# Kernel optimization log

Hardware: AMD Instinct MI355X
Metric: run time of the kernel (lower is better)

The kernel has to match this reference:

```python
import jax, jax.numpy as jnp
import numpy as np

EMBED_DIM = 1024
HID = EMBED_DIM // 2
N = 32768
L2_REG = 0.001
BN_EPS = 1e-5


def setup_inputs() -> dict:
    key = jax.random.key(0)
    ks = jax.random.split(key, 8)
    inp = {
        "item_emb": jax.random.normal(ks[0], (N, EMBED_DIM), jnp.float32),
        "pos_item_emb": jax.random.normal(ks[1], (N, EMBED_DIM), jnp.float32),
        "neg_item_emb": jax.random.normal(ks[2], (N, EMBED_DIM), jnp.float32),
        # Linear 1: embed_dim -> embed_dim/2 (xavier_normal init, zero bias)
        "W1": jax.random.normal(ks[3], (HID, EMBED_DIM), jnp.float32) * np.sqrt(2.0 / (EMBED_DIM + HID)),
        "b1": jnp.zeros((HID,), jnp.float32),
        # BatchNorm1d params / running stats (eval-mode semantics)
        "gamma": jnp.ones((HID,), jnp.float32),
        "beta": jnp.zeros((HID,), jnp.float32),
        "run_mean": jnp.zeros((HID,), jnp.float32),
        "run_var": jnp.ones((HID,), jnp.float32),
        # Linear 2: embed_dim/2 -> embed_dim
        "W2": jax.random.normal(ks[4], (EMBED_DIM, HID), jnp.float32) * np.sqrt(2.0 / (EMBED_DIM + HID)),
        "b2": jnp.zeros((EMBED_DIM,), jnp.float32),
    }
    return inp


def _net(x, W1, b1, gamma, beta, run_mean, run_var, W2, b2):
    # Linear -> BatchNorm1d (eval stats) -> LeakyReLU(0.1) -> (Dropout=identity) -> Linear
    h = x @ W1.T + b1                                   # [N, HID]
    h = (h - run_mean) * jax.lax.rsqrt(run_var + BN_EPS) * gamma + beta
    h = jnp.where(h >= 0, h, 0.1 * h)
    return h @ W2.T + b2                                # [N, EMBED_DIM]


def reference(item_emb, pos_item_emb, neg_item_emb,
              W1, b1, gamma, beta, run_mean, run_var, W2, b2):
    net = lambda x: _net(x, W1, b1, gamma, beta, run_mean, run_var, W2, b2)
    anchor_e = net(item_emb)
    pos_e = net(pos_item_emb)
    neg_e = net(neg_item_emb)

    dist_pos = jnp.linalg.norm(anchor_e - pos_e, axis=1)  # [N]
    dist_neg = jnp.linalg.norm(anchor_e - neg_e, axis=1)  # [N]

    # fused replacement of the per-sample python loop
    margins = jnp.where(dist_neg < dist_pos, dist_pos - dist_neg, 0.0)
    margin = jnp.quantile(margins, 0.25)  # Q1, linear interpolation (matches torch)

    loss_triplet = jax.nn.relu(dist_neg ** 2 - dist_pos ** 2 + margin)
    l2 = L2_REG * (jnp.sum(anchor_e ** 2) + jnp.sum(pos_e ** 2) + jnp.sum(neg_e ** 2)) / anchor_e.shape[0]
    return jnp.mean(loss_triplet + l2)
```

## Files before the change

kernel.cpp:

```cpp
#include <hip/hip_runtime.h>

#define NROWS 32768
#define DIM   1024
#define HIDD  512
#define M3    (3*NROWS)

using bf16x8 = __attribute__((ext_vector_type(8))) short;
using f32x4  = __attribute__((ext_vector_type(4))) float;

#define MFMA16(a,b,c) __builtin_amdgcn_mfma_f32_16x16x32_bf16(a,b,c,0,0,0)
#define WAIT_VM(N)  asm volatile("s_waitcnt vmcnt(" #N ")" ::: "memory")
#define WAIT_LGKM0  asm volatile("s_waitcnt lgkmcnt(0)" ::: "memory")
#define MEMFENCE    asm volatile("" ::: "memory")
#define BAR()       __builtin_amdgcn_s_barrier()
#define SCHEDB()    __builtin_amdgcn_sched_barrier(0)
#define SP1()       __builtin_amdgcn_s_setprio(1)
#define SP0()       __builtin_amdgcn_s_setprio(0)

static __device__ __forceinline__ unsigned short f2bf(float f) {
    unsigned u = __float_as_uint(f);
    u += 0x7FFFu + ((u >> 16) & 1u);
    return (unsigned short)(u >> 16);
}
static __device__ __forceinline__ unsigned cvtpk(float a, float b) {
    unsigned r;
    asm("v_cvt_pk_bf16_f32 %0, %1, %2" : "=v"(r) : "v"(a), "v"(b));
    return r;
}
static __device__ __forceinline__ void gload16(const void* gsrc, void* ldst) {
    __builtin_amdgcn_global_load_lds(
        (const __attribute__((address_space(1))) unsigned int*)gsrc,
        (__attribute__((address_space(3))) unsigned int*)ldst,
        16, 0, 0);
}

__global__ __launch_bounds__(256)
void cvt_kernel(const float* __restrict__ src, unsigned short* __restrict__ dst, int n4)
{
    const int i = blockIdx.x * 256 + threadIdx.x;
    if (i < n4) {
        float4 v = reinterpret_cast<const float4*>(src)[i];
        uint2 o;
        o.x = cvtpk(v.x, v.y);
        o.y = cvtpk(v.z, v.w);
        reinterpret_cast<uint2*>(dst)[i] = o;
    }
}

__global__ __launch_bounds__(512, 1)
void gemm1_mfma(const float* __restrict__ x0, const float* __restrict__ x1,
                const float* __restrict__ x2,
                const unsigned short* __restrict__ W1bf,
                const float* __restrict__ b1, const float* __restrict__ gamma,
                const float* __restrict__ beta, const float* __restrict__ rmean,
                const float* __restrict__ rvar,
                unsigned short* __restrict__ h)
{
    __shared__ char smem[131072];
    char* const Ab = smem;
    char* const Bb = smem + 65536;

    const int lin = blockIdx.x;
    const int wgid = (lin & 7) * 96 + (lin >> 3);
    const int cb = wgid & 1;
    const int rb = wgid >> 1;
    const int tid  = threadIdx.x;
    const int lane = tid & 63, w = tid >> 6;
    const int wm = w >> 2, wn = w & 3;
    const int row0 = rb * 256;
    const int s = row0 >> 15;
    const float* x = (s == 0) ? x0 : (s == 1 ? x1 : x2);
    const int rl0 = row0 & (NROWS - 1);
    const int col0 = cb * 256;
    const int l15 = lane & 15, lq = lane >> 4;

    f32x4 acc[8][4] = {};
    float4 aR[8];

    const int arow = tid >> 1, ahalf = tid & 1;
    const float* axsrc = &x[(size_t)(rl0 + arow) * DIM + ahalf * 32];

    auto issueA = [&](int k0) {
        #pragma unroll
        for (int j = 0; j < 8; ++j)
            aR[j] = *reinterpret_cast<const float4*>(axsrc + k0 + j * 4);
    };
    auto issueB = [&](int k0, char* Bdst) {
        #pragma unroll
        for (int i = 0; i < 4; ++i) {
            const int f = i * 512 + tid;
            const int col = f >> 3, c = f & 7;
            gload16(&W1bf[(size_t)(col0 + col) * DIM + k0 + ((c ^ (col & 7)) << 3)],
                    Bdst + f * 16);
        }
    };
    auto writeA = [&](char* Adst) {
        #pragma unroll
        for (int j = 0; j < 4; ++j) {
            uint4 o;
            o.x = cvtpk(aR[2*j].x, aR[2*j].y);
            o.y = cvtpk(aR[2*j].z, aR[2*j].w);
            o.z = cvtpk(aR[2*j+1].x, aR[2*j+1].y);
            o.w = cvtpk(aR[2*j+1].z, aR[2*j+1].w);
            const int cidx = ahalf * 4 + j;
            *reinterpret_cast<uint4*>(Adst + ((arow * 128 + cidx * 16) ^ ((arow & 7) << 4))) = o;
        }
    };
    auto readA = [&](bf16x8 (&a)[4][2], int mh, char* Abase) {
        #pragma unroll
        for (int mm = 0; mm < 4; ++mm) {
            const int row = wm * 128 + (mh * 4 + mm) * 16 + l15;
            const int swz = (row & 7) << 4;
            #pragma unroll
            for (int ks = 0; ks < 2; ++ks)
                a[mm][ks] = *reinterpret_cast<const bf16x8*>(
                    Abase + ((row * 128 + ks * 64 + lq * 16) ^ swz));
        }
    };
    auto readB = [&](bf16x8 (&b)[2][2], int nh, char* Bbase) {
        #pragma unroll
        for (int nn = 0; nn < 2; ++nn) {
            const int col = wn * 64 + (nh * 2 + nn) * 16 + l15;
            const int swz = (col & 7) << 4;
            #pragma unroll
            for (int ks = 0; ks < 2; ++ks)
                b[nn][ks] = *reinterpret_cast<const bf16x8*>(
                    Bbase + ((col * 128 + ks * 64 + lq * 16) ^ swz));
        }
    };

    issueA(0);
    MEMFENCE;
    issueB(0, Bb);
    WAIT_VM(4);
    writeA(Ab);
    WAIT_VM(0);
    WAIT_LGKM0;
    BAR();

    for (int t = 0; t < 16; ++t) {
        char* const Apt = Ab + (t & 1) * 32768;
        char* const Apn = Ab + ((t & 1) ^ 1) * 32768;
        char* const Bpt = Bb + (t & 1) * 32768;
        char* const Bpn = Bb + ((t & 1) ^ 1) * 32768;
        const int kn = ((t < 15) ? (t + 1) : 15) * 64;

        bf16x8 a[4][2], b[2][2], a2[4][2];
        readA(a, 0, Apt);
        readB(b, 0, Bpt);
        issueA(kn);
        MEMFENCE;
        issueB(kn, Bpn);
        BAR(); WAIT_LGKM0; SCHEDB(); SP1();
        #pragma unroll
        for (int mm = 0; mm < 4; ++mm)
            #pragma unroll
            for (int nn = 0; nn < 2; ++nn)
                #pragma unroll
                for (int ks = 0; ks < 2; ++ks)
                    acc[mm][nn] = MFMA16(a[mm][ks], b[nn][ks], acc[mm][nn]);
        SP0(); BAR();
        readB(b, 1, Bpt);
        BAR(); WAIT_LGKM0; SCHEDB(); SP1();
        #pragma unroll
        for (int mm = 0; mm < 4; ++mm)
            #pragma unroll
            for (int nn = 0; nn < 2; ++nn)
                #pragma unroll
                for (int ks = 0; ks < 2; ++ks)
                    acc[mm][2 + nn] = MFMA16(a[mm][ks], b[nn][ks], acc[mm][2 + nn]);
        SP0(); BAR();
        readA(a2, 1, Apt);
        WAIT_VM(4);
        writeA(Apn);
        BAR(); WAIT_LGKM0; SCHEDB(); SP1();
        #pragma unroll
        for (int mm = 0; mm < 4; ++mm)
            #pragma unroll
            for (int nn = 0; nn < 2; ++nn)
                #pragma unroll
                for (int ks = 0; ks < 2; ++ks)
                    acc[4 + mm][2 + nn] = MFMA16(a2[mm][ks], b[nn][ks], acc[4 + mm][2 + nn]);
        SP0(); BAR();
        readB(b, 0, Bpt);
        WAIT_VM(0);
        BAR(); WAIT_LGKM0; SCHEDB(); SP1();
        #pragma unroll
        for (int mm = 0; mm < 4; ++mm)
            #pragma unroll
            for (int nn = 0; nn < 2; ++nn)
                #pragma unroll
                for (int ks = 0; ks < 2; ++ks)
                    acc[4 + mm][nn] = MFMA16(a2[mm][ks], b[nn][ks], acc[4 + mm][nn]);
        SP0(); BAR();
    }

    float Asc[4], Bsc[4];
    #pragma unroll
    for (int nf = 0; nf < 4; ++nf) {
        const int c = col0 + wn * 64 + nf * 16 + l15;
        const float inv = rsqrtf(rvar[c] + 1e-5f);
        Asc[nf] = inv * gamma[c];
        Bsc[nf] = (b1[c] - rmean[c]) * Asc[nf] + beta[c];
    }
    #pragma unroll
    for (int mf = 0; mf < 8; ++mf) {
        const int rbase = row0 + wm * 128 + mf * 16 + lq * 4;
        #pragma unroll
        for (int nf = 0; nf < 4; ++nf) {
            const int c = col0 + wn * 64 + nf * 16 + l15;
            #pragma unroll
            for (int i = 0; i < 4; ++i) {
                float v = fmaf(acc[mf][nf][i], Asc[nf], Bsc[nf]);
                v = (v >= 0.f) ? v : 0.1f * v;
                h[(size_t)(rbase + i) * HIDD + c] = f2bf(v);
            }
        }
    }
}

__global__ __launch_bounds__(512, 1)
void gemm2_mfma(const unsigned short* __restrict__ h,
                const unsigned short* __restrict__ W2bf,
                const float* __restrict__ b2,
                float* __restrict__ pdp, float* __restrict__ pdn,
                float* __restrict__ pl2)
{
    __shared__ char smem[114688];
    char* const Ab = smem;
    char* const Bb = smem + 49152;

    const int lin = blockIdx.x;
    const int wgid = (lin & 7) * 256 + (lin >> 3);
    const int cb = wgid & 3;
    const int rb = wgid >> 2;
    const int tid  = threadIdx.x;
    const int lane = tid & 63, w = tid >> 6;
    const int wm = w >> 2, wn = w & 3;
    const int row0 = rb * 64;
    const int col0 = cb * 256;
    const int l15 = lane & 15, lq = lane >> 4;

    f32x4 acc[6][4] = {};

    auto issueA = [&](int k0, char* Adst) {
        #pragma unroll
        for (int i = 0; i < 3; ++i) {
            const int f = i * 512 + tid;
            const int mrow = f >> 3, c = f & 7;
            const int mf = mrow >> 4, rr = mrow & 15;
            const int ss = mf % 3, rf = mf / 3;
            gload16(&h[((size_t)ss * NROWS + row0 + rf * 16 + rr) * HIDD + k0 + ((c ^ (mrow & 7)) << 3)],
                    Adst + f * 16);
        }
    };
    auto issueB = [&](int k0, char* Bdst) {
        #pragma unroll
        for (int i = 0; i < 4; ++i) {
            const int f = i * 512 + tid;
            const int col = f >> 3, c = f & 7;
            gload16(&W2bf[(size_t)(col0 + col) * HIDD + k0 + ((c ^ (col & 7)) << 3)],
                    Bdst + f * 16);
        }
    };
    auto readA = [&](bf16x8 (&a)[3][2], int mh, char* Abase) {
        #pragma unroll
        for (int mm = 0; mm < 3; ++mm) {
            const int row = (wm * 6 + mh * 3 + mm) * 16 + l15;
            const int swz = (row & 7) << 4;
            #pragma unroll
            for (int ks = 0; ks < 2; ++ks)
                a[mm][ks] = *reinterpret_cast<const bf16x8*>(
                    Abase + ((row * 128 + ks * 64 + lq * 16) ^ swz));
        }
    };
    auto readB = [&](bf16x8 (&b)[2][2], int nh, char* Bbase) {
        #pragma unroll
        for (int nn = 0; nn < 2; ++nn) {
            const int col = wn * 64 + (nh * 2 + nn) * 16 + l15;
            const int swz = (col & 7) << 4;
            #pragma unroll
            for (int ks = 0; ks < 2; ++ks)
                b[nn][ks] = *reinterpret_cast<const bf16x8*>(
                    Bbase + ((col * 128 + ks * 64 + lq * 16) ^ swz));
        }
    };

    issueA(0, Ab);
    MEMFENCE;
    issueB(0, Bb);
    WAIT_VM(0);
    BAR();

    for (int t = 0; t < 8; ++t) {
        char* const Apt = Ab + (t & 1) * 24576;
        char* const Apn = Ab + ((t & 1) ^ 1) * 24576;
        char* const Bpt = Bb + (t & 1) * 32768;
        char* const Bpn = Bb + ((t & 1) ^ 1) * 32768;
        const int kn = ((t < 7) ? (t + 1) : 7) * 64;

        bf16x8 a[3][2], b[2][2], a2[3][2];
        readA(a, 0, Apt);
        readB(b, 0, Bpt);
        issueA(kn, Apn);
        MEMFENCE;
        issueB(kn, Bpn);
        BAR(); WAIT_LGKM0; SCHEDB(); SP1();
        #pragma unroll
        for (int mm = 0; mm < 3; ++mm)
            #pragma unroll
            for (int nn = 0; nn < 2; ++nn)
                #pragma unroll
                for (int ks = 0; ks < 2; ++ks)
                    acc[mm][nn] = MFMA16(a[mm][ks], b[nn][ks], acc[mm][nn]);
        SP0(); BAR();
        readB(b, 1, Bpt);
        BAR(); WAIT_LGKM0; SCHEDB(); SP1();
        #pragma unroll
        for (int mm = 0; mm < 3; ++mm)
            #pragma unroll
            for (int nn = 0; nn < 2; ++nn)
                #pragma unroll
                for (int ks = 0; ks < 2; ++ks)
                    acc[mm][2 + nn] = MFMA16(a[mm][ks], b[nn][ks], acc[mm][2 + nn]);
        SP0(); BAR();
        readA(a2, 1, Apt);
        BAR(); WAIT_LGKM0; SCHEDB(); SP1();
        #pragma unroll
        for (int mm = 0; mm < 3; ++mm)
            #pragma unroll
            for (int nn = 0; nn < 2; ++nn)
                #pragma unroll
                for (int ks = 0; ks < 2; ++ks)
                    acc[3 + mm][2 + nn] = MFMA16(a2[mm][ks], b[nn][ks], acc[3 + mm][2 + nn]);
        SP0(); BAR();
        readB(b, 0, Bpt);
        WAIT_VM(0);
        BAR(); WAIT_LGKM0; SCHEDB(); SP1();
        #pragma unroll
        for (int mm = 0; mm < 3; ++mm)
            #pragma unroll
            for (int nn = 0; nn < 2; ++nn)
                #pragma unroll
                for (int ks = 0; ks < 2; ++ks)
                    acc[3 + mm][nn] = MFMA16(a2[mm][ks], b[nn][ks], acc[3 + mm][nn]);
        SP0(); BAR();
    }

    float b2c[4];
    #pragma unroll
    for (int nf = 0; nf < 4; ++nf) b2c[nf] = b2[col0 + wn * 64 + nf * 16 + l15];
    float l2t = 0.f;
    #pragma unroll
    for (int mh = 0; mh < 2; ++mh) {
        const int rbase = row0 + (wm * 2 + mh) * 16 + lq * 4;
        #pragma unroll
        for (int i = 0; i < 4; ++i) {
            float dp = 0.f, dn = 0.f;
            #pragma unroll
            for (int nf = 0; nf < 4; ++nf) {
                const float ea = acc[mh * 3 + 0][nf][i] + b2c[nf];
                const float ep = acc[mh * 3 + 1][nf][i] + b2c[nf];
                const float en = acc[mh * 3 + 2][nf][i] + b2c[nf];
                dp += (ea - ep) * (ea - ep);
                dn += (ea - en) * (ea - en);
                l2t += ea * ea + ep * ep + en * en;
            }
            #pragma unroll
            for (int mm = 1; mm < 16; mm <<= 1) {
                dp += __shfl_xor(dp, mm);
                dn += __shfl_xor(dn, mm);
            }
            if (l15 == 0) {
                pdp[(size_t)(cb * 4 + wn) * NROWS + rbase + i] = dp;
                pdn[(size_t)(cb * 4 + wn) * NROWS + rbase + i] = dn;
            }
        }
    }
    #pragma unroll
    for (int mm = 1; mm < 64; mm <<= 1) l2t += __shfl_xor(l2t, mm);
    __syncthreads();
    float* const l2red = (float*)smem;
    if (lane == 0) l2red[w] = l2t;
    __syncthreads();
    if (tid == 0) {
        float t = 0.f;
        #pragma unroll
        for (int ww = 0; ww < 8; ++ww) t += l2red[ww];
        pl2[wgid] = t;
    }
}

__global__ __launch_bounds__(256)
void margins_kernel(const float* __restrict__ pdp, const float* __restrict__ pdn,
                    float* __restrict__ margins, float* __restrict__ dd)
{
    const int r = blockIdx.x * 256 + threadIdx.x;
    float dp2 = 0.f, dn2 = 0.f;
    #pragma unroll
    for (int q = 0; q < 16; ++q) {
        dp2 += pdp[(size_t)q * NROWS + r];
        dn2 += pdn[(size_t)q * NROWS + r];
    }
    dd[r] = dn2 - dp2;
    margins[r] = (dn2 < dp2) ? (sqrtf(dp2) - sqrtf(dn2)) : 0.f;
}

__global__ __launch_bounds__(1024)
void final_kernel(const float* __restrict__ pl2, int npl2,
                  const float* __restrict__ margins, const float* __restrict__ dd,
                  float* __restrict__ out)
{
    __shared__ unsigned hist[256];
    __shared__ float warp_red[16];
    __shared__ unsigned sh_prefix;
    __shared__ int sh_k;
    __shared__ float sh_l2;
    const int tid = threadIdx.x;

    float l2 = 0.f;
    for (int i = tid; i < npl2; i += 1024) l2 += pl2[i];
    #pragma unroll
    for (int m = 1; m < 64; m <<= 1) l2 += __shfl_xor(l2, m);
    if ((tid & 63) == 0) warp_red[tid >> 6] = l2;
    __syncthreads();
    if (tid == 0) {
        float t = 0.f;
        for (int w = 0; w < 16; ++w) t += warp_red[w];
        sh_l2 = t;
    }
    __syncthreads();

    float vsel[2];
    for (int sel = 0; sel < 2; ++sel) {
        if (tid == 0) { sh_k = 8191 + sel; sh_prefix = 0u; }
        __syncthreads();
        for (int shift = 24; shift >= 0; shift -= 8) {
            if (tid < 256) hist[tid] = 0u;
            __syncthreads();
            const unsigned prefix = sh_prefix;
            const unsigned mask = (shift == 24) ? 0u : (0xFFFFFFFFu << (shift + 8));
            for (int i = tid; i < NROWS; i += 1024) {
                const unsigned key = __float_as_uint(margins[i]);
                if (((key ^ prefix) & mask) == 0u)
                    atomicAdd(&hist[(key >> shift) & 255u], 1u);
            }
            __syncthreads();
            if (tid == 0) {
                int kk = sh_k;
                unsigned cum = 0; int d = 0;
                for (; d < 256; ++d) {
                    const unsigned c = hist[d];
                    if (cum + c > (unsigned)kk) break;
                    cum += c;
                }
                sh_prefix = prefix | ((unsigned)d << shift);
                sh_k = kk - (int)cum;
            }
            __syncthreads();
        }
        vsel[sel] = __uint_as_float(sh_prefix);
        __syncthreads();
    }
    const float margin = vsel[0] + 0.75f * (vsel[1] - vsel[0]);

    float ssum = 0.f;
    for (int i = tid; i < NROWS; i += 1024) {
        const float t = dd[i] + margin;
        ssum += (t > 0.f) ? t : 0.f;
    }
    #pragma unroll
    for (int m = 1; m < 64; m <<= 1) ssum += __shfl_xor(ssum, m);
    if ((tid & 63) == 0) warp_red[tid >> 6] = ssum;
    __syncthreads();
    if (tid == 0) {
        float S = 0.f;
        for (int w = 0; w < 16; ++w) S += warp_red[w];
        out[0] = S / (float)NROWS + 1e-3f * sh_l2 / (float)NROWS;
    }
}

extern "C" void kernel_launch(void* const* d_in, const int* in_sizes, int n_in,
                              void* d_out, int out_size, void* d_ws, size_t ws_size,
                              hipStream_t stream) {
    (void)in_sizes; (void)n_in; (void)out_size; (void)ws_size;
    const float* item = (const float*)d_in[0];
    const float* pos  = (const float*)d_in[1];
    const float* neg  = (const float*)d_in[2];
    const float* W1   = (const float*)d_in[3];
    const float* b1   = (const float*)d_in[4];
    const float* gam  = (const float*)d_in[5];
    const float* bet  = (const float*)d_in[6];
    const float* rmu  = (const float*)d_in[7];
    const float* rvr  = (const float*)d_in[8];
    const float* W2   = (const float*)d_in[9];
    const float* b2   = (const float*)d_in[10];

    char* ws = (char*)d_ws;
    unsigned short* h = (unsigned short*)ws;
    size_t off = (size_t)M3 * HIDD * sizeof(unsigned short);
    unsigned short* W1bf = (unsigned short*)(ws + off); off += (size_t)HIDD * DIM * 2;
    unsigned short* W2bf = (unsigned short*)(ws + off); off += (size_t)DIM * HIDD * 2;
    float* pdp = (float*)(ws + off); off += (size_t)16 * NROWS * 4;
    float* pdn = (float*)(ws + off); off += (size_t)16 * NROWS * 4;
    float* pl2 = (float*)(ws + off); off += (size_t)2048 * 4;
    float* margins = (float*)(ws + off); off += (size_t)NROWS * 4;
    float* dd = (float*)(ws + off); off += (size_t)NROWS * 4;

    cvt_kernel<<<dim3((HIDD*DIM/4 + 255)/256), 256, 0, stream>>>(W1, W1bf, HIDD*DIM/4);
    cvt_kernel<<<dim3((DIM*HIDD/4 + 255)/256), 256, 0, stream>>>(W2, W2bf, DIM*HIDD/4);
    gemm1_mfma<<<dim3(768), 512, 0, stream>>>(
        item, pos, neg, W1bf, b1, gam, bet, rmu, rvr, h);
    gemm2_mfma<<<dim3(2048), 512, 0, stream>>>(
        h, W2bf, b2, pdp, pdn, pl2);
    margins_kernel<<<dim3(NROWS/256), 256, 0, stream>>>(pdp, pdn, margins, dd);
    final_kernel<<<1, 1024, 0, stream>>>(pl2, 2048, margins, dd, (float*)d_out);
}
```

Before: 501.9 us.

## Shrink GEMM1 tiles to 128x128 with 256 threads and single-pass quantile selection

GEMM1 moves from a 256x256 tile with 512 threads, 128KB double-buffered LDS and an interleaved MFMA schedule to a 128x128 tile with 256 threads, 32KB single-buffered LDS and register prefetch of the next X slice. The operands are swapped so the epilogue writes packed bf16 pairs after reading BN scale/shift from LDS. The aim is higher occupancy and simpler sync, but A/B reuse per block drops and the explicit load/compute overlap is gone. Separately, the final kernel finds the second order statistic for the quantile with one count/min pass instead of a second 4-pass radix select.

Result: faster. 438.9 us (-12.6%).

```diff
diff --git a/kernel.cpp b/kernel.cpp
--- a/kernel.cpp
+++ b/kernel.cpp
@@ -17,11 +17,6 @@
 #define SP1()       __builtin_amdgcn_s_setprio(1)
 #define SP0()       __builtin_amdgcn_s_setprio(0)
 
-static __device__ __forceinline__ unsigned short f2bf(float f) {
-    unsigned u = __float_as_uint(f);
-    u += 0x7FFFu + ((u >> 16) & 1u);
-    return (unsigned short)(u >> 16);
-}
 static __device__ __forceinline__ unsigned cvtpk(float a, float b) {
     unsigned r;
     asm("v_cvt_pk_bf16_f32 %0, %1, %2" : "=v"(r) : "v"(a), "v"(b));
@@ -47,7 +42,7 @@
     }
 }
 
-__global__ __launch_bounds__(512, 1)
+__global__ __launch_bounds__(256)
 void gemm1_mfma(const float* __restrict__ x0, const float* __restrict__ x1,
                 const float* __restrict__ x2,
                 const unsigned short* __restrict__ W1bf,
@@ -56,165 +51,117 @@
                 const float* __restrict__ rvar,
                 unsigned short* __restrict__ h)
 {
-    __shared__ char smem[131072];
-    char* const Ab = smem;
-    char* const Bb = smem + 65536;
+    __shared__ char smem[32768];
+    char* const Xb = smem;
+    char* const Wb = smem + 16384;
 
     const int lin = blockIdx.x;
-    const int wgid = (lin & 7) * 96 + (lin >> 3);
-    const int cb = wgid & 1;
-    const int rb = wgid >> 1;
+    const int wgid = (lin & 7) * 384 + (lin >> 3);
+    const int cb = wgid & 3;
+    const int rb = wgid >> 2;
     const int tid  = threadIdx.x;
     const int lane = tid & 63, w = tid >> 6;
-    const int wm = w >> 2, wn = w & 3;
-    const int row0 = rb * 256;
+    const int wr = w >> 1, wc = w & 1;
+    const int row0 = rb * 128;
     const int s = row0 >> 15;
     const float* x = (s == 0) ? x0 : (s == 1 ? x1 : x2);
     const int rl0 = row0 & (NROWS - 1);
-    const int col0 = cb * 256;
+    const int col0 = cb * 128;
     const int l15 = lane & 15, lq = lane >> 4;
 
-    f32x4 acc[8][4] = {};
+    f32x4 acc[4][4] = {};
     float4 aR[8];
 
-    const int arow = tid >> 1, ahalf = tid & 1;
-    const float* axsrc = &x[(size_t)(rl0 + arow) * DIM + ahalf * 32];
-
-    auto issueA = [&](int k0) {
-        #pragma unroll
-        for (int j = 0; j < 8; ++j)
-            aR[j] = *reinterpret_cast<const float4*>(axsrc + k0 + j * 4);
-    };
-    auto issueB = [&](int k0, char* Bdst) {
-        #pragma unroll
-        for (int i = 0; i < 4; ++i) {
-            const int f = i * 512 + tid;
-            const int col = f >> 3, c = f & 7;
-            gload16(&W1bf[(size_t)(col0 + col) * DIM + k0 + ((c ^ (col & 7)) << 3)],
-                    Bdst + f * 16);
-        }
-    };
-    auto writeA = [&](char* Adst) {
-        #pragma unroll
-        for (int j = 0; j < 4; ++j) {
-            uint4 o;
-            o.x = cvtpk(aR[2*j].x, aR[2*j].y);
-            o.y = cvtpk(aR[2*j].z, aR[2*j].w);
-            o.z = cvtpk(aR[2*j+1].x, aR[2*j+1].y);
-            o.w = cvtpk(aR[2*j+1].z, aR[2*j+1].w);
-            const int cidx = ahalf * 4 + j;
-            *reinterpret_cast<uint4*>(Adst + ((arow * 128 + cidx * 16) ^ ((arow & 7) << 4))) = o;
-        }
-    };
-    auto readA = [&](bf16x8 (&a)[4][2], int mh, char* Abase) {
-        #pragma unroll
-        for (int mm = 0; mm < 4; ++mm) {
-            const int row = wm * 128 + (mh * 4 + mm) * 16 + l15;
-            const int swz = (row & 7) << 4;
-            #pragma unroll
-            for (int ks = 0; ks < 2; ++ks)
-                a[mm][ks] = *reinterpret_cast<const bf16x8*>(
-                    Abase + ((row * 128 + ks * 64 + lq * 16) ^ swz));
-        }
-    };
-    auto readB = [&](bf16x8 (&b)[2][2], int nh, char* Bbase) {
-        #pragma unroll
-        for (int nn = 0; nn < 2; ++nn) {
-            const int col = wn * 64 + (nh * 2 + nn) * 16 + l15;
-            const int swz = (col & 7) << 4;
-            #pragma unroll
-            for (int ks = 0; ks < 2; ++ks)
-                b[nn][ks] = *reinterpret_cast<const bf16x8*>(
-                    Bbase + ((col * 128 + ks * 64 + lq * 16) ^ swz));
-        }
-    };
-
-    issueA(0);
-    MEMFENCE;
-    issueB(0, Bb);
-    WAIT_VM(4);
-    writeA(Ab);
-    WAIT_VM(0);
-    WAIT_LGKM0;
-    BAR();
+    #pragma unroll
+    for (int p = 0; p < 8; ++p) {
+        const int f = p * 256 + tid;
+        const int r = f >> 4, c4 = f & 15;
+        aR[p] = *reinterpret_cast<const float4*>(&x[(size_t)(rl0 + r) * DIM + c4 * 4]);
+    }
 
     for (int t = 0; t < 16; ++t) {
-        char* const Apt = Ab + (t & 1) * 32768;
-        char* const Apn = Ab + ((t & 1) ^ 1) * 32768;
-        char* const Bpt = Bb + (t & 1) * 32768;
-        char* const Bpn = Bb + ((t & 1) ^ 1) * 32768;
-        const int kn = ((t < 15) ? (t + 1) : 15) * 64;
-
-        bf16x8 a[4][2], b[2][2], a2[4][2];
-        readA(a, 0, Apt);
-        readB(b, 0, Bpt);
-        issueA(kn);
-        MEMFENCE;
-        issueB(kn, Bpn);
-        BAR(); WAIT_LGKM0; SCHEDB(); SP1();
-        #pragma unroll
-        for (int mm = 0; mm < 4; ++mm)
-            #pragma unroll
-            for (int nn = 0; nn < 2; ++nn)
+        const int k0 = t * 64;
+        #pragma unroll
+        for (int p = 0; p < 8; ++p) {
+            const int f = p * 256 + tid;
+            const int r = f >> 4, c4 = f & 15;
+            const unsigned off = (unsigned)((r * 128 + c4 * 8) ^ ((r & 7) << 4));
+            uint2 o; o.x = cvtpk(aR[p].x, aR[p].y); o.y = cvtpk(aR[p].z, aR[p].w);
+            *reinterpret_cast<uint2*>(Xb + off) = o;
+        }
+        #pragma unroll
+        for (int c = 0; c < 4; ++c) {
+            const int f = c * 256 + tid;
+            const int panel = f >> 9;
+            const int cc = (f >> 2) & 127;
+            const int chunk = (f & 3) ^ ((cc >> 1) & 3);
+            gload16(&W1bf[(size_t)(col0 + cc) * DIM + k0 + panel * 32 + chunk * 8],
+                    Wb + (size_t)f * 16);
+        }
+        __syncthreads();
+        if (t < 15) {
+            #pragma unroll
+            for (int p = 0; p < 8; ++p) {
+                const int f = p * 256 + tid;
+                const int r = f >> 4, c4 = f & 15;
+                aR[p] = *reinterpret_cast<const float4*>(
+                    &x[(size_t)(rl0 + r) * DIM + k0 + 64 + c4 * 4]);
+            }
+        }
+        bf16x8 wf[2][4], xf[2][4];
+        #pragma unroll
+        for (int kk = 0; kk < 2; ++kk) {
+            #pragma unroll
+            for (int cf = 0; cf < 4; ++cf) {
+                const int colr = wc * 64 + cf * 16 + l15;
+                const int slq = lq ^ ((colr >> 1) & 3);
+                wf[kk][cf] = *reinterpret_cast<const bf16x8*>(Wb + kk * 8192 + colr * 64 + slq * 16);
+            }
+            #pragma unroll
+            for (int rf = 0; rf < 4; ++rf) {
+                const int row = wr * 64 + rf * 16 + l15;
+                xf[kk][rf] = *reinterpret_cast<const bf16x8*>(
+                    Xb + ((row * 128 + kk * 64 + lq * 16) ^ ((row & 7) << 4)));
+            }
+        }
+        #pragma unroll
+        for (int kk = 0; kk < 2; ++kk)
+            #pragma unroll
+            for (int cf = 0; cf < 4; ++cf)
                 #pragma unroll
-                for (int ks = 0; ks < 2; ++ks)
-                    acc[mm][nn] = MFMA16(a[mm][ks], b[nn][ks], acc[mm][nn]);
-        SP0(); BAR();
-        readB(b, 1, Bpt);
-        BAR(); WAIT_LGKM0; SCHEDB(); SP1();
-        #pragma unroll
-        for (int mm = 0; mm < 4; ++mm)
-            #pragma unroll
-            for (int nn = 0; nn < 2; ++nn)
-                #pragma unroll
-                for (int ks = 0; ks < 2; ++ks)
-                    acc[mm][2 + nn] = MFMA16(a[mm][ks], b[nn][ks], acc[mm][2 + nn]);
-        SP0(); BAR();
-        readA(a2, 1, Apt);
-        WAIT_VM(4);
-        writeA(Apn);
-        BAR(); WAIT_LGKM0; SCHEDB(); SP1();
-        #pragma unroll
-        for (int mm = 0; mm < 4; ++mm)
-            #pragma unroll
-            for (int nn = 0; nn < 2; ++nn)
-                #pragma unroll
-                for (int ks = 0; ks < 2; ++ks)
-                    acc[4 + mm][2 + nn] = MFMA16(a2[mm][ks], b[nn][ks], acc[4 + mm][2 + nn]);
-        SP0(); BAR();
-        readB(b, 0, Bpt);
-        WAIT_VM(0);
-        BAR(); WAIT_LGKM0; SCHEDB(); SP1();
-        #pragma unroll
-        for (int mm = 0; mm < 4; ++mm)
-            #pragma unroll
-            for (int nn = 0; nn < 2; ++nn)
-                #pragma unroll
-                for (int ks = 0; ks < 2; ++ks)
-                    acc[4 + mm][nn] = MFMA16(a2[mm][ks], b[nn][ks], acc[4 + mm][nn]);
-        SP0(); BAR();
-    }
-
-    float Asc[4], Bsc[4];
-    #pragma unroll
-    for (int nf = 0; nf < 4; ++nf) {
-        const int c = col0 + wn * 64 + nf * 16 + l15;
-        const float inv = rsqrtf(rvar[c] + 1e-5f);
-        Asc[nf] = inv * gamma[c];
-        Bsc[nf] = (b1[c] - rmean[c]) * Asc[nf] + beta[c];
-    }
-    #pragma unroll
-    for (int mf = 0; mf < 8; ++mf) {
-        const int rbase = row0 + wm * 128 + mf * 16 + lq * 4;
-        #pragma unroll
-        for (int nf = 0; nf < 4; ++nf) {
-            const int c = col0 + wn * 64 + nf * 16 + l15;
-            #pragma unroll
-            for (int i = 0; i < 4; ++i) {
-                float v = fmaf(acc[mf][nf][i], Asc[nf], Bsc[nf]);
-                v = (v >= 0.f) ? v : 0.1f * v;
-                h[(size_t)(rbase + i) * HIDD + c] = f2bf(v);
-            }
+                for (int rf = 0; rf < 4; ++rf)
+                    acc[cf][rf] = MFMA16(wf[kk][cf], xf[kk][rf], acc[cf][rf]);
+        __syncthreads();
+    }
+
+    float2* const sAB = (float2*)smem;
+    if (tid < 128) {
+        const int c = col0 + tid;
+        const float a = rsqrtf(rvar[c] + 1e-5f) * gamma[c];
+        sAB[tid] = make_float2(a, (b1[c] - rmean[c]) * a + beta[c]);
+    }
+    __syncthreads();
+
+    #pragma unroll
+    for (int cf = 0; cf < 4; ++cf) {
+        const int cbase = wc * 64 + cf * 16 + lq * 4;
+        const float2 ab0 = sAB[cbase + 0];
+        const float2 ab1 = sAB[cbase + 1];
+        const float2 ab2 = sAB[cbase + 2];
+        const float2 ab3 = sAB[cbase + 3];
+        #pragma unroll
+        for (int rf = 0; rf < 4; ++rf) {
+            const int r = row0 + wr * 64 + rf * 16 + l15;
+            float v0 = fmaf(acc[cf][rf][0], ab0.x, ab0.y);
+            float v1 = fmaf(acc[cf][rf][1], ab1.x, ab1.y);
+            float v2 = fmaf(acc[cf][rf][2], ab2.x, ab2.y);
+            float v3 = fmaf(acc[cf][rf][3], ab3.x, ab3.y);
+            v0 = (v0 >= 0.f) ? v0 : 0.1f * v0;
+            v1 = (v1 >= 0.f) ? v1 : 0.1f * v1;
+            v2 = (v2 >= 0.f) ? v2 : 0.1f * v2;
+            v3 = (v3 >= 0.f) ? v3 : 0.1f * v3;
+            uint2 o; o.x = cvtpk(v0, v1); o.y = cvtpk(v2, v3);
+            *reinterpret_cast<uint2*>(&h[(size_t)r * HIDD + col0 + cbase]) = o;
         }
     }
 }
@@ -416,6 +363,8 @@
     __shared__ unsigned sh_prefix;
     __shared__ int sh_k;
     __shared__ float sh_l2;
+    __shared__ unsigned sh_cle;
+    __shared__ unsigned sh_minAbove;
     const int tid = threadIdx.x;
 
     float l2 = 0.f;
@@ -428,41 +377,55 @@
         float t = 0.f;
         for (int w = 0; w < 16; ++w) t += warp_red[w];
         sh_l2 = t;
-    }
-    __syncthreads();
-
-    float vsel[2];
-    for (int sel = 0; sel < 2; ++sel) {
-        if (tid == 0) { sh_k = 8191 + sel; sh_prefix = 0u; }
+        sh_k = 8191; sh_prefix = 0u;
+        sh_cle = 0u; sh_minAbove = 0xFFFFFFFFu;
+    }
+    __syncthreads();
+
+    for (int shift = 24; shift >= 0; shift -= 8) {
+        if (tid < 256) hist[tid] = 0u;
         __syncthreads();
-        for (int shift = 24; shift >= 0; shift -= 8) {
-            if (tid < 256) hist[tid] = 0u;
-            __syncthreads();
-            const unsigned prefix = sh_prefix;
-            const unsigned mask = (shift == 24) ? 0u : (0xFFFFFFFFu << (shift + 8));
-            for (int i = tid; i < NROWS; i += 1024) {
-                const unsigned key = __float_as_uint(margins[i]);
-                if (((key ^ prefix) & mask) == 0u)
-                    atomicAdd(&hist[(key >> shift) & 255u], 1u);
-            }
-            __syncthreads();
-            if (tid == 0) {
-                int kk = sh_k;
-                unsigned cum = 0; int d = 0;
-                for (; d < 256; ++d) {
-                    const unsigned c = hist[d];
-                    if (cum + c > (unsigned)kk) break;
-                    cum += c;
-                }
-                sh_prefix = prefix | ((unsigned)d << shift);
-                sh_k = kk - (int)cum;
-            }
-            __syncthreads();
-        }
-        vsel[sel] = __uint_as_float(sh_prefix);
+        const unsigned prefix = sh_prefix;
+        const unsigned mask = (shift == 24) ? 0u : (0xFFFFFFFFu << (shift + 8));
+        for (int i = tid; i < NROWS; i += 1024) {
+            const unsigned key = __float_as_uint(margins[i]);
+            if (((key ^ prefix) & mask) == 0u)
+                atomicAdd(&hist[(key >> shift) & 255u], 1u);
+        }
         __syncthreads();
-    }
-    const float margin = vsel[0] + 0.75f * (vsel[1] - vsel[0]);
+        if (tid == 0) {
+            int kk = sh_k;
+            unsigned cum = 0; int d = 0;
+            for (; d < 256; ++d) {
+                const unsigned c = hist[d];
+                if (cum + c > (unsigned)kk) break;
+                cum += c;
+            }
+            sh_prefix = prefix | ((unsigned)d << shift);
+            sh_k = kk - (int)cum;
+        }
+        __syncthreads();
+    }
+    const unsigned p1u = sh_prefix;
+
+    unsigned lc = 0, lmin = 0xFFFFFFFFu;
+    for (int i = tid; i < NROWS; i += 1024) {
+        const unsigned key = __float_as_uint(margins[i]);
+        if (key <= p1u) ++lc; else lmin = min(lmin, key);
+    }
+    #pragma unroll
+    for (int m = 1; m < 64; m <<= 1) {
+        lc += __shfl_xor(lc, m);
+        lmin = min(lmin, (unsigned)__shfl_xor((int)lmin, m));
+    }
+    if ((tid & 63) == 0) {
+        atomicAdd(&sh_cle, lc);
+        atomicMin(&sh_minAbove, lmin);
+    }
+    __syncthreads();
+    const float p1 = __uint_as_float(p1u);
+    const float p2 = (sh_cle >= 8193u) ? p1 : __uint_as_float(sh_minAbove);
+    const float margin = p1 + 0.75f * (p2 - p1);
 
     float ssum = 0.f;
     for (int i = tid; i < NROWS; i += 1024) {
@@ -509,7 +472,7 @@
 
     cvt_kernel<<<dim3((HIDD*DIM/4 + 255)/256), 256, 0, stream>>>(W1, W1bf, HIDD*DIM/4);
     cvt_kernel<<<dim3((DIM*HIDD/4 + 255)/256), 256, 0, stream>>>(W2, W2bf, DIM*HIDD/4);
-    gemm1_mfma<<<dim3(768), 512, 0, stream>>>(
+    gemm1_mfma<<<dim3(3072), 256, 0, stream>>>(
         item, pos, neg, W1bf, b1, gam, bet, rmu, rvr, h);
     gemm2_mfma<<<dim3(2048), 512, 0, stream>>>(
         h, W2bf, b2, pdp, pdn, pl2);
```
